# Kernel optimization log

Measured on AMD Instinct MI355X. Metric: run time of the kernel, lower is better.

## Reference

```python
import jax, jax.numpy as jnp
import numpy as np
import math

EPS = 1e-5
NUM_HEADS = 8

def _ln(x, g, b):
    m = x.mean(-1, keepdims=True)
    v = ((x - m) ** 2).mean(-1, keepdims=True)
    return (x - m) / jnp.sqrt(v + EPS) * g + b

def _swish(x):
    return x * jax.nn.sigmoid(x)

def _rope(x):
    # lucidrains RotaryEmbedding.rotate_queries_or_keys: rotates along axis -2,
    # interleaved pair convention, base 10000.
    n, d = x.shape[-2], x.shape[-1]
    inv = 1.0 / (10000.0 ** (jnp.arange(0, d, 2, dtype=jnp.float32) / d))
    freqs = jnp.arange(n, dtype=jnp.float32)[:, None] * inv[None, :]  # (n, d/2)
    cos = jnp.repeat(jnp.cos(freqs), 2, axis=-1)  # (n, d)
    sin = jnp.repeat(jnp.sin(freqs), 2, axis=-1)
    x1, x2 = x[..., 0::2], x[..., 1::2]
    rot = jnp.stack([-x2, x1], axis=-1).reshape(x.shape)
    return x * cos + rot * sin

def _ffn(x, w1, b1, w2, b2):
    # FeedForwardModule: x + 0.5 * (Linear -> Swish -> Linear)
    return x + 0.5 * (_swish(x @ w1 + b1) @ w2 + b2)

def _mhsa(x, g, b, wq, bq, wk, bk, wv, bv, wo, bo):
    B, T, D = x.shape
    dh = D // NUM_HEADS
    y = _ln(x, g, b)
    q = (y @ wq + bq).reshape(B, T, NUM_HEADS, dh)                         # (b,t,h,d)
    k = (y @ wk + bk).reshape(B, T, NUM_HEADS, dh).transpose(0, 2, 1, 3)   # (b,h,t,d)
    v = (y @ wv + bv).reshape(B, T, NUM_HEADS, dh).transpose(0, 2, 1, 3)
    # Faithful to source: query is NOT permuted before rotary, so RoPE acts on
    # axis -2 which is heads for q and time for k (matches torch code exactly).
    q = _rope(q).transpose(0, 2, 1, 3)                                     # (b,h,t,d)
    k = _rope(k)
    score = jnp.einsum('bhtd,bhsd->bhts', q, k) / math.sqrt(D)             # /sqrt(d_model)
    attn = jax.nn.softmax(score, axis=-1)
    ctx = jnp.einsum('bhts,bhsd->bhtd', attn, v).transpose(0, 2, 1, 3).reshape(B, T, D)
    return x + ctx @ wo + bo

def _conv_module(x, g, b, pw1_w, pw1_b, dw_w, dw_b, bn_g, bn_b, pw2_w, pw2_b):
    C = dw_w.shape[-1]  # 2*dim
    y = _ln(x, g, b)
    y = jnp.einsum('btd,ed->bte', y, pw1_w) + pw1_b            # pointwise conv (b,t,4*dim)
    a, gate = y[..., :C], y[..., C:]
    y = a * jax.nn.sigmoid(gate)                                # GLU over channel dim
    y = jax.lax.conv_general_dilated(
        y, dw_w, window_strides=(1,), padding='SAME',
        dimension_numbers=('NWC', 'WIO', 'NWC'), feature_group_count=C) + dw_b
    m = y.mean(axis=(0, 1))                                     # BatchNorm1d, training stats
    v = ((y - m) ** 2).mean(axis=(0, 1))
    y = (y - m) / jnp.sqrt(v + EPS) * bn_g + bn_b
    y = _swish(y)
    y = jnp.einsum('btc,dc->btd', y, pw2_w) + pw2_b             # pointwise conv back to dim
    return x + y

def setup_inputs():
    key = jax.random.key(0)
    B, T, D, K = 8, 1024, 512, 31
    HID = 2 * D
    C = 2 * D
    ks = jax.random.split(key, 16)
    rn = lambda k, shp: jax.random.normal(k, shp, jnp.float32) * 0.02
    zeros = lambda n: jnp.zeros((n,), jnp.float32)
    ones = lambda n: jnp.ones((n,), jnp.float32)
    return dict(
        x=jax.random.normal(ks[0], (B, T, D), jnp.float32),
        ffn1_w1=rn(ks[1], (D, HID)), ffn1_b1=zeros(HID),
        ffn1_w2=rn(ks[2], (HID, D)), ffn1_b2=zeros(D),
        ln_attn_g=ones(D), ln_attn_b=zeros(D),
        wq=rn(ks[3], (D, D)), bq=zeros(D),
        wk=rn(ks[4], (D, D)), bk=zeros(D),
        wv=rn(ks[5], (D, D)), bv=zeros(D),
        wo=rn(ks[6], (D, D)), bo=zeros(D),
        conv_ln_g=ones(D), conv_ln_b=zeros(D),
        pw1_w=rn(ks[7], (2 * C, D)), pw1_b=zeros(2 * C),
        dw_w=rn(ks[8], (K, 1, C)), dw_b=zeros(C),
        bn_g=ones(C), bn_b=zeros(C),
        pw2_w=rn(ks[9], (D, C)), pw2_b=zeros(D),
        ffn2_w1=rn(ks[10], (D, HID)), ffn2_b1=zeros(HID),
        ffn2_w2=rn(ks[11], (HID, D)), ffn2_b2=zeros(D),
        ln_out_g=ones(D), ln_out_b=zeros(D),
    )

def reference(x, ffn1_w1, ffn1_b1, ffn1_w2, ffn1_b2, ln_attn_g, ln_attn_b,
              wq, bq, wk, bk, wv, bv, wo, bo,
              conv_ln_g, conv_ln_b, pw1_w, pw1_b, dw_w, dw_b, bn_g, bn_b, pw2_w, pw2_b,
              ffn2_w1, ffn2_b1, ffn2_w2, ffn2_b2, ln_out_g, ln_out_b):
    y = _ffn(x, ffn1_w1, ffn1_b1, ffn1_w2, ffn1_b2)
    y = _mhsa(y, ln_attn_g, ln_attn_b, wq, bq, wk, bk, wv, bv, wo, bo)
    y = _conv_module(y, conv_ln_g, conv_ln_b, pw1_w, pw1_b, dw_w, dw_b, bn_g, bn_b, pw2_w, pw2_b)
    y = _ffn(y, ffn2_w1, ffn2_b1, ffn2_w2, ffn2_b2)
    return _ln(y, ln_out_g, ln_out_b)
```

## Files before the change

### kernel.cpp

```cpp
#include <hip/hip_runtime.h>
#include <hip/hip_bf16.h>


#define M_ROWS 8192

using bf16x8 = __attribute__((ext_vector_type(8))) short;
using f32x4  = __attribute__((ext_vector_type(4))) float;
using s8v    = __attribute__((ext_vector_type(8))) short;
using s4v    = __attribute__((ext_vector_type(4))) short;

__device__ __forceinline__ float sigmoid_(float v) { return 1.f / (1.f + expf(-v)); }

__device__ __forceinline__ float bf2f(short s) {
  return __uint_as_float(((unsigned)(unsigned short)s) << 16);
}
__device__ __forceinline__ short f2bf(float f) {
  unsigned u = __float_as_uint(f);
  unsigned r = (u + 0x7fffu + ((u >> 16) & 1u)) >> 16;
  return (short)r;
}

__device__ __forceinline__ void gl16(const void* g, void* l) {
  __builtin_amdgcn_global_load_lds((const __attribute__((address_space(1))) void*)g,
                                   (__attribute__((address_space(3))) void*)l, 16, 0, 0);
}

template <int BM, int BN, int BK, int EPI>
__global__ __launch_bounds__(256) void mgemm(
    const short* __restrict__ A, const short* __restrict__ Bt,
    const float* __restrict__ bias, const float* __restrict__ res,
    const short* __restrict__ resb, short* __restrict__ outb, int M, int N, int K) {
  constexpr int WR = BM / 64;
  constexpr int WC = 4 / WR;
  constexpr int NF = BN / (16 * WC);
  constexpr int KH = BK / 32;
  constexpr int APASS = (BM * BK) / 2048;
  constexpr int BPASS = (BN * BK) / 2048;
  constexpr int RPP = 2048 / BK;
  constexpr int LPS = APASS + BPASS;
  __shared__ __align__(16) short As[2][BM * BK];
  __shared__ __align__(16) short Bs[2][BN * BK];
  __shared__ __align__(16) short vstg[EPI == 4 ? 64 * 132 : 1];
  const int tid = threadIdx.x;
  const int lane = tid & 63, wid = tid >> 6;
  const int wr = wid / WC, wc = wid % WC;
  const int nbx = gridDim.x;
  const int nwg = nbx * gridDim.y;
  int id = blockIdx.y * nbx + blockIdx.x;
  id = (id & 7) * (nwg >> 3) + (id >> 3);
  const int bm = (id / nbx) * BM;
  const int bn = (id % nbx) * BN;
  f32x4 acc[4][NF];
#pragma unroll
  for (int m = 0; m < 4; ++m)
#pragma unroll
    for (int n = 0; n < NF; ++n) acc[m][n] = (f32x4){0.f, 0.f, 0.f, 0.f};
  const short* Ablk = A + (size_t)bm * K;
  const short* Bblk = Bt + (size_t)bn * K;
  const int jl = tid & (BK / 8 - 1);
  const int r0 = tid / (BK / 8);
  const int ks = ((BK == 64) ? (jl ^ (r0 & 7)) : jl) << 3;
#define STAGE(buf, k0)                                                                 \
  do {                                                                                 \
    _Pragma("unroll")                                                                  \
    for (int p = 0; p < APASS; ++p)                                                    \
      gl16(Ablk + (size_t)(r0 + p * RPP) * K + (k0) + ks,                              \
           (char*)As[buf] + p * 4096 + wid * 1024);                                    \
    _Pragma("unroll")                                                                  \
    for (int p = 0; p < BPASS; ++p)                                                    \
      gl16(Bblk + (size_t)(r0 + p * RPP) * K + (k0) + ks,                              \
           (char*)Bs[buf] + p * 4096 + wid * 1024);                                    \
  } while (0)

  STAGE(0, 0);
  STAGE(1, BK);
  const int NS = K / BK;
  const int fr = lane & 15, fg = lane >> 4;
  const int arow = wr * 64 + fr;
  const int brow = wc * (BN / WC) + fr;
  for (int i = 0; i < NS; ++i) {
    if (i + 1 < NS) {
      if constexpr (LPS == 4)      asm volatile("s_waitcnt vmcnt(4)" ::: "memory");
      else if constexpr (LPS == 3) asm volatile("s_waitcnt vmcnt(3)" ::: "memory");
      else                         asm volatile("s_waitcnt vmcnt(2)" ::: "memory");
    } else {
      asm volatile("s_waitcnt vmcnt(0)" ::: "memory");
    }
    __builtin_amdgcn_s_barrier();
    asm volatile("" ::: "memory");
    const int cur = i & 1;
    bf16x8 af[KH][4], bfr[KH][NF];
#pragma unroll
    for (int kk = 0; kk < KH; ++kk) {
      const int cx = (BK == 64) ? (((((kk << 2) + fg)) ^ (fr & 7)) << 3)
                                : ((fg << 3) + kk * 32);
#pragma unroll
      for (int m = 0; m < 4; ++m)
        af[kk][m] = *reinterpret_cast<const bf16x8*>(&As[cur][(arow + m * 16) * BK + cx]);
#pragma unroll
      for (int n = 0; n < NF; ++n)
        bfr[kk][n] = *reinterpret_cast<const bf16x8*>(&Bs[cur][(brow + n * 16) * BK + cx]);
    }
    asm volatile("s_waitcnt lgkmcnt(0)" ::: "memory");
    __builtin_amdgcn_s_barrier();
    if ((i + 2) * BK < K) STAGE(cur, (i + 2) * BK);
#pragma unroll
    for (int kk = 0; kk < KH; ++kk)
#pragma unroll
      for (int m = 0; m < 4; ++m)
#pragma unroll
        for (int n = 0; n < NF; ++n)
          acc[m][n] = __builtin_amdgcn_mfma_f32_16x16x32_bf16(af[kk][m], bfr[kk][n],
                                                              acc[m][n], 0, 0, 0);
  }
#undef STAGE
  const int orow0 = bm + wr * 64 + ((lane >> 4) << 2);
  const int ocol0 = bn + wc * (BN / WC) + fr;

  if constexpr (EPI == 4) {
    const int sel = bn >> 9;
    const float2* tbl = (const float2*)res;
    if (sel == 2) {
      const int b_ = bm >> 10, t0v = bm & 1023;
      const int hb = (bn & 511) >> 6;
#pragma unroll
      for (int pass = 0; pass < 2; ++pass) {
        __syncthreads();
        if (wc == pass) {
#pragma unroll
          for (int m = 0; m < 4; ++m) {
            const int rl = wr * 64 + ((lane >> 4) << 2) + m * 16;
#pragma unroll
            for (int n = 0; n < NF; ++n) {
              const int dl = fr + n * 16;
              const float bv = bias[bn + wc * 64 + dl];
#pragma unroll
              for (int r = 0; r < 4; ++r)
                vstg[dl * 132 + rl + r] = f2bf(acc[m][n][r] + bv);
            }
          }
        }
        __syncthreads();
#pragma unroll
        for (int it = 0; it < 4; ++it) {
          const int c = tid + (it << 8);
          const int d = c >> 4, t8 = (c & 15) << 3;
          const s8v val = *reinterpret_cast<const s8v*>(&vstg[d * 132 + t8]);
          *reinterpret_cast<s8v*>(
              &outb[(size_t)8388608 + (((size_t)((b_ << 3) + hb + pass)) << 16) +
                    ((size_t)d << 10) + t0v + t8]) = val;
        }
      }
    } else {
      const float qsc = (sel == 0) ? 0.04419417382415922f : 1.f;
#pragma unroll
      for (int n = 0; n < NF; ++n) {
        const int col = ocol0 + n * 16;
        const int h = (col >> 6) & 7, d = col & 63;
        const int p = d >> 1;
        const float bv = bias[col];
#pragma unroll
        for (int m = 0; m < 4; ++m) {
#pragma unroll
          for (int r = 0; r < 4; ++r) {
            const int row = orow0 + m * 16 + r;
            const int b_ = row >> 10, t_ = row & 1023;
            const int pos = (sel == 0) ? h : t_;
            const float2 cs = tbl[pos * 32 + p];
            float vv = acc[m][n][r] + bv;
            const float pv = __shfl_xor(vv, 1);
            float o = ((lane & 1) == 0) ? (vv * cs.x - pv * cs.y) : (vv * cs.x + pv * cs.y);
            outb[(size_t)sel * 4194304 + (((size_t)((b_ << 3) + h)) << 16) + ((size_t)t_ << 6) + d] =
                f2bf(o * qsc);
          }
        }
      }
    }
  } else if constexpr (EPI == 6) {
    const int j = bn >> 7;
#pragma unroll
    for (int m = 0; m < 4; ++m) {
#pragma unroll
      for (int np = 0; np < NF / 2; ++np) {
        const int gc = (j << 6) + ((wc * 2 + np) << 4) + fr;
        const float ba = bias[gc];
        const float bg = bias[1024 + gc];
#pragma unroll
        for (int r = 0; r < 4; ++r) {
          const int row = orow0 + m * 16 + r;
          const float a = acc[m][2 * np][r] + ba;
          const float g = acc[m][2 * np + 1][r] + bg;
          outb[(size_t)row * 1024 + gc] = f2bf(a * sigmoid_(g));
        }
      }
    }
  } else {
#pragma unroll
    for (int m = 0; m < 4; ++m) {
#pragma unroll
      for (int n = 0; n < NF; ++n) {
        const int col = ocol0 + n * 16;
        const float bv = bias[col];
#pragma unroll
        for (int r = 0; r < 4; ++r) {
          const int row = orow0 + m * 16 + r;
          float v = acc[m][n][r] + bv;
          if constexpr (EPI == 1) {
            v = v * sigmoid_(v);
          } else if constexpr (EPI == 2) {
            v += bf2f(resb[(size_t)row * N + col]);
          } else if constexpr (EPI == 3) {
            v = bf2f(resb[(size_t)row * N + col]) + 0.5f * v;
          }
          outb[(size_t)row * N + col] = f2bf(v);
        }
      }
    }
  }
}

__device__ __forceinline__ void dev_cast8(const float* in, short* out, int i) {
  const float4 a = *reinterpret_cast<const float4*>(&in[(size_t)i * 8]);
  const float4 b = *reinterpret_cast<const float4*>(&in[(size_t)i * 8 + 4]);
  s8v o = { f2bf(a.x), f2bf(a.y), f2bf(a.z), f2bf(a.w),
            f2bf(b.x), f2bf(b.y), f2bf(b.z), f2bf(b.w) };
  *reinterpret_cast<s8v*>(&out[(size_t)i * 8]) = o;
}

__global__ __launch_bounds__(256) void prep_kernel(
    const float* __restrict__ x, short* __restrict__ xb,
    const float* __restrict__ f1w1, short* __restrict__ wf1w1,
    const float* __restrict__ f1w2, short* __restrict__ wf1w2,
    const float* __restrict__ wq, const float* __restrict__ wk,
    const float* __restrict__ wv, short* __restrict__ wqkv,
    const float* __restrict__ wo, short* __restrict__ wwo,
    const float* __restrict__ pw1, short* __restrict__ wpw1,
    const float* __restrict__ pw2, short* __restrict__ wpw2,
    const float* __restrict__ f2w1, short* __restrict__ wf2w1,
    const float* __restrict__ f2w2, short* __restrict__ wf2w2,
    const float* __restrict__ bq, const float* __restrict__ bk,
    const float* __restrict__ bv, float* __restrict__ bqkv,
    float* __restrict__ rtbl) {
  __shared__ float t[32][33];
  const int blk = blockIdx.x, tid = threadIdx.x;
  const float* tin = nullptr;
  short* tout = nullptr;
  int tK = 0, tN = 0, tr = 0, tnbx = 0;
  if (blk < 2048) {
    dev_cast8(x, xb, blk * 256 + tid);
    return;
  } else if (blk < 2560) { tin = f1w1; tout = wf1w1; tK = 512; tN = 1024; tr = blk - 2048; tnbx = 32; }
  else if (blk < 3072)   { tin = f1w2; tout = wf1w2; tK = 1024; tN = 512; tr = blk - 2560; tnbx = 16; }
  else if (blk < 3328)   { tin = wq; tout = wqkv; tK = 512; tN = 512; tr = blk - 3072; tnbx = 16; }
  else if (blk < 3584)   { tin = wk; tout = wqkv + 512 * 512; tK = 512; tN = 512; tr = blk - 3328; tnbx = 16; }
  else if (blk < 3840)   { tin = wv; tout = wqkv + 1024 * 512; tK = 512; tN = 512; tr = blk - 3584; tnbx = 16; }
  else if (blk < 4096)   { tin = wo; tout = wwo; tK = 512; tN = 512; tr = blk - 3840; tnbx = 16; }
  else if (blk < 4608) {
    const int idx = (blk - 4096) * 256 + tid;
    const int pc = idx >> 6, kk = (idx & 63) << 3;
    const int j = pc >> 7, s = (pc >> 4) & 7, fr = pc & 15;
    const int oc = ((s & 1) << 10) + (j << 6) + ((s >> 1) << 4) + fr;
    const float4 a = *reinterpret_cast<const float4*>(&pw1[(size_t)oc * 512 + kk]);
    const float4 b = *reinterpret_cast<const float4*>(&pw1[(size_t)oc * 512 + kk + 4]);
    s8v o = { f2bf(a.x), f2bf(a.y), f2bf(a.z), f2bf(a.w),
              f2bf(b.x), f2bf(b.y), f2bf(b.z), f2bf(b.w) };
    *reinterpret_cast<s8v*>(&wpw1[(size_t)pc * 512 + kk]) = o;
    return;
  } else if (blk < 4864) {
    dev_cast8(pw2, wpw2, (blk - 4608) * 256 + tid);
    return;
  } else if (blk < 5376) { tin = f2w1; tout = wf2w1; tK = 512; tN = 1024; tr = blk - 4864; tnbx = 32; }
  else if (blk < 5888)   { tin = f2w2; tout = wf2w2; tK = 1024; tN = 512; tr = blk - 5376; tnbx = 16; }
  else if (blk < 6016) {
    const int i = (blk - 5888) * 256 + tid;
    const int tt = i >> 5, p = i & 31;
    const float inv = exp2f(-(float)p * 0.41524101186092f);
    float s, c;
    sincosf((float)tt * inv, &s, &c);
    rtbl[i * 2] = c;
    rtbl[i * 2 + 1] = s;
    return;
  } else {
    const int i = (blk - 6016) * 256 + tid;
    if (i < 1536) bqkv[i] = i < 512 ? bq[i] : (i < 1024 ? bk[i - 512] : bv[i - 1024]);
    return;
  }
  const int n0 = (tr % tnbx) << 5, k0 = (tr / tnbx) << 5;
  const int tx = tid & 31, ty = tid >> 5;
  for (int r = ty; r < 32; r += 8) t[r][tx] = tin[(size_t)(k0 + r) * tN + n0 + tx];
  __syncthreads();
  for (int r = ty; r < 32; r += 8) tout[(size_t)(n0 + r) * tK + k0 + tx] = f2bf(t[tx][r]);
}

template <typename OT>
__global__ __launch_bounds__(256) void ln_kernel(
    const short* __restrict__ in, const float* __restrict__ g,
    const float* __restrict__ b, OT* __restrict__ out) {
  __shared__ float sm[4];
  const size_t row = blockIdx.x;
  const int tid = threadIdx.x;
  const short* x = in + (row << 9);
  const int pr = *reinterpret_cast<const int*>(&x[tid << 1]);
  const float v0 = bf2f((short)(pr & 0xffff));
  const float v1 = bf2f((short)(((unsigned)pr) >> 16));
  float s = v0 + v1;
  for (int o = 32; o; o >>= 1) s += __shfl_xor(s, o);
  if ((tid & 63) == 0) sm[tid >> 6] = s;
  __syncthreads();
  const float mean = (sm[0] + sm[1] + sm[2] + sm[3]) * (1.f / 512.f);
  __syncthreads();
  const float d0 = v0 - mean, d1 = v1 - mean;
  float q = d0 * d0 + d1 * d1;
  for (int o = 32; o; o >>= 1) q += __shfl_xor(q, o);
  if ((tid & 63) == 0) sm[tid >> 6] = q;
  __syncthreads();
  const float var = (sm[0] + sm[1] + sm[2] + sm[3]) * (1.f / 512.f);
  const float inv = rsqrtf(var + 1e-5f);
  const float2 gv = *reinterpret_cast<const float2*>(&g[tid << 1]);
  const float2 bv = *reinterpret_cast<const float2*>(&b[tid << 1]);
  const float o0 = d0 * inv * gv.x + bv.x;
  const float o1 = d1 * inv * gv.y + bv.y;
  if constexpr (sizeof(OT) == 2) {
    const int pk = (int)(unsigned short)f2bf(o0) | ((int)(unsigned short)f2bf(o1) << 16);
    *reinterpret_cast<int*>(&out[(row << 9) + (tid << 1)]) = pk;
  } else {
    float2 o = {o0, o1};
    *reinterpret_cast<float2*>(&out[(row << 9) + (tid << 1)]) = o;
  }
}

__global__ __launch_bounds__(256) void attn_mfma_kernel(
    const short* __restrict__ q, const short* __restrict__ k,
    const short* __restrict__ vt, short* __restrict__ ctx) {
  __shared__ __align__(16) short Qs[64][72];
  __shared__ __align__(16) short Ks[64][72];
  __shared__ __align__(16) short VsT[64][72];
  __shared__ __align__(16) short Ps[64][72];
  const int bx = ((blockIdx.x & 7) << 7) | (blockIdx.x >> 3);
  const int bh = bx >> 4, qt = bx & 15;
  const int b_ = bh >> 3, h_ = bh & 7;
  const int tid = threadIdx.x, lane = tid & 63, w = tid >> 6;
  const int t0 = qt << 6;
  const short* qbase = q + ((size_t)bh << 16) + ((size_t)t0 << 6);
  const short* kbase = k + ((size_t)bh << 16);
  const short* vtbase = vt + ((size_t)bh << 16);
  const int sr = tid >> 2, scg = (tid & 3) << 4;
  {
    const s8v a = *reinterpret_cast<const s8v*>(&qbase[(size_t)sr * 64 + scg]);
    const s8v b = *reinterpret_cast<const s8v*>(&qbase[(size_t)sr * 64 + scg + 8]);
    *reinterpret_cast<s8v*>(&Qs[sr][scg]) = a;
    *reinterpret_cast<s8v*>(&Qs[sr][scg + 8]) = b;
    const s8v k0a = *reinterpret_cast<const s8v*>(&kbase[(size_t)sr * 64 + scg]);
    const s8v k0b = *reinterpret_cast<const s8v*>(&kbase[(size_t)sr * 64 + scg + 8]);
    *reinterpret_cast<s8v*>(&Ks[sr][scg]) = k0a;
    *reinterpret_cast<s8v*>(&Ks[sr][scg + 8]) = k0b;
    const s8v v0a = *reinterpret_cast<const s8v*>(&vtbase[((size_t)sr << 10) + scg]);
    const s8v v0b = *reinterpret_cast<const s8v*>(&vtbase[((size_t)sr << 10) + scg + 8]);
    *reinterpret_cast<s8v*>(&VsT[sr][scg]) = v0a;
    *reinterpret_cast<s8v*>(&VsT[sr][scg + 8]) = v0b;
  }
  __syncthreads();
  const int fr = lane & 15, fg = lane >> 4;
  const int koff0 = fg << 3;
  bf16x8 qf[2];
  qf[0] = *reinterpret_cast<const bf16x8*>(&Qs[w * 16 + fr][koff0]);
  qf[1] = *reinterpret_cast<const bf16x8*>(&Qs[w * 16 + fr][32 + koff0]);
  float m[4] = {-1e30f, -1e30f, -1e30f, -1e30f};
  float l[4] = {0.f, 0.f, 0.f, 0.f};
  f32x4 outv[4];
#pragma unroll
  for (int n = 0; n < 4; ++n) outv[n] = (f32x4){0.f, 0.f, 0.f, 0.f};

  for (int i = 0; i < 16; ++i) {
    s8v nk0, nk1, nv0, nv1;
    const bool pf = (i < 15);
    if (pf) {
      const int kn = (i + 1) << 6;
      nk0 = *reinterpret_cast<const s8v*>(&kbase[(size_t)(kn + sr) * 64 + scg]);
      nk1 = *reinterpret_cast<const s8v*>(&kbase[(size_t)(kn + sr) * 64 + scg + 8]);
      nv0 = *reinterpret_cast<const s8v*>(&vtbase[((size_t)sr << 10) + kn + scg]);
      nv1 = *reinterpret_cast<const s8v*>(&vtbase[((size_t)sr << 10) + kn + scg + 8]);
    }
    f32x4 sacc[4];
    __builtin_amdgcn_s_setprio(1);
#pragma unroll
    for (int n = 0; n < 4; ++n) {
      sacc[n] = (f32x4){0.f, 0.f, 0.f, 0.f};
      const bf16x8 kf0 = *reinterpret_cast<const bf16x8*>(&Ks[n * 16 + fr][koff0]);
      const bf16x8 kf1 = *reinterpret_cast<const bf16x8*>(&Ks[n * 16 + fr][32 + koff0]);
      sacc[n] = __builtin_amdgcn_mfma_f32_16x16x32_bf16(qf[0], kf0, sacc[n], 0, 0, 0);
      sacc[n] = __builtin_amdgcn_mfma_f32_16x16x32_bf16(qf[1], kf1, sacc[n], 0, 0, 0);
    }
    __builtin_amdgcn_s_setprio(0);
    float vm[4];
#pragma unroll
    for (int r = 0; r < 4; ++r)
      vm[r] = fmaxf(fmaxf(sacc[0][r], sacc[1][r]), fmaxf(sacc[2][r], sacc[3][r]));
    const bool ok = vm[0] <= m[0] + 8.f && vm[1] <= m[1] + 8.f &&
                    vm[2] <= m[2] + 8.f && vm[3] <= m[3] + 8.f;
    if (__all(ok)) {
#pragma unroll
      for (int r = 0; r < 4; ++r) {
        const float p0 = __expf(sacc[0][r] - m[r]), p1 = __expf(sacc[1][r] - m[r]);
        const float p2 = __expf(sacc[2][r] - m[r]), p3 = __expf(sacc[3][r] - m[r]);
        l[r] += p0 + p1 + p2 + p3;
        const int qr = w * 16 + (fg << 2) + r;
        Ps[qr][fr] = f2bf(p0);
        Ps[qr][16 + fr] = f2bf(p1);
        Ps[qr][32 + fr] = f2bf(p2);
        Ps[qr][48 + fr] = f2bf(p3);
      }
    } else {
#pragma unroll
      for (int r = 0; r < 4; ++r) {
        float rm = vm[r];
        rm = fmaxf(rm, __shfl_xor(rm, 1));
        rm = fmaxf(rm, __shfl_xor(rm, 2));
        rm = fmaxf(rm, __shfl_xor(rm, 4));
        rm = fmaxf(rm, __shfl_xor(rm, 8));
        const float nm = fmaxf(m[r], rm);
        const float al = __expf(m[r] - nm);
        m[r] = nm;
        const float p0 = __expf(sacc[0][r] - nm), p1 = __expf(sacc[1][r] - nm);
        const float p2 = __expf(sacc[2][r] - nm), p3 = __expf(sacc[3][r] - nm);
        l[r] = l[r] * al + (p0 + p1 + p2 + p3);
        outv[0][r] *= al; outv[1][r] *= al; outv[2][r] *= al; outv[3][r] *= al;
        const int qr = w * 16 + (fg << 2) + r;
        Ps[qr][fr] = f2bf(p0);
        Ps[qr][16 + fr] = f2bf(p1);
        Ps[qr][32 + fr] = f2bf(p2);
        Ps[qr][48 + fr] = f2bf(p3);
      }
    }
    __syncthreads();
    if (pf) {
      *reinterpret_cast<s8v*>(&Ks[sr][scg]) = nk0;
      *reinterpret_cast<s8v*>(&Ks[sr][scg + 8]) = nk1;
    }
    const bf16x8 pa0 = *reinterpret_cast<const bf16x8*>(&Ps[w * 16 + fr][koff0]);
    const bf16x8 pa1 = *reinterpret_cast<const bf16x8*>(&Ps[w * 16 + fr][32 + koff0]);
    __builtin_amdgcn_s_setprio(1);
#pragma unroll
    for (int n = 0; n < 4; ++n) {
      const bf16x8 vf0 = *reinterpret_cast<const bf16x8*>(&VsT[n * 16 + fr][koff0]);
      const bf16x8 vf1 = *reinterpret_cast<const bf16x8*>(&VsT[n * 16 + fr][32 + koff0]);
      outv[n] = __builtin_amdgcn_mfma_f32_16x16x32_bf16(pa0, vf0, outv[n], 0, 0, 0);
      outv[n] = __builtin_amdgcn_mfma_f32_16x16x32_bf16(pa1, vf1, outv[n], 0, 0, 0);
    }
    __builtin_amdgcn_s_setprio(0);
    __syncthreads();
    if (pf) {
      *reinterpret_cast<s8v*>(&VsT[sr][scg]) = nv0;
      *reinterpret_cast<s8v*>(&VsT[sr][scg + 8]) = nv1;
    }
  }
#pragma unroll
  for (int r = 0; r < 4; ++r) {
    float L = l[r];
    L += __shfl_xor(L, 1);
    L += __shfl_xor(L, 2);
    L += __shfl_xor(L, 4);
    L += __shfl_xor(L, 8);
    const float inv = 1.f / L;
    const int t = t0 + w * 16 + (fg << 2) + r;
    const size_t base = (((size_t)((b_ << 10) | t)) << 9) + (h_ << 6);
#pragma unroll
    for (int n = 0; n < 4; ++n)
      ctx[base + n * 16 + fr] = f2bf(outv[n][r] * inv);
  }
}

__global__ __launch_bounds__(256) void dwconv_kernel(
    const short* __restrict__ in, const float* __restrict__ w,
    const float* __restrict__ bias, short* __restrict__ out) {
  __shared__ __align__(16) short tile[286 * 72];
  __shared__ float wlds[31 * 64];
  const int id = blockIdx.x;
  const int ct = id & 15, tt = (id >> 4) & 3;
  const size_t b = id >> 6;
  const int c0 = ct << 6, t0 = tt << 8;
  const int tid = threadIdx.x;
  for (int i = tid; i < 31 * 64; i += 256) {
    const int kk = i >> 6, c = i & 63;
    wlds[i] = w[kk * 1024 + c0 + c];
  }
  for (int i = tid; i < 286 * 8; i += 256) {
    const int row = i >> 3, seg = i & 7;
    const int gt = t0 - 15 + row;
    s8v val = {};
    if (gt >= 0 && gt < 1024)
      val = *reinterpret_cast<const s8v*>(&in[(b << 20) + ((size_t)gt << 10) + c0 + (seg << 3)]);
    *reinterpret_cast<s8v*>(&tile[row * 72 + (seg << 3)]) = val;
  }
  __syncthreads();
  const int cg = tid & 7, tg = tid >> 3;
  const int tl = tg << 3;
  float acc[8][8];
  const float4 b0 = *reinterpret_cast<const float4*>(&bias[c0 + (cg << 3)]);
  const float4 b1 = *reinterpret_cast<const float4*>(&bias[c0 + (cg << 3) + 4]);
#pragma unroll
  for (int t = 0; t < 8; ++t) {
    acc[t][0] = b0.x; acc[t][1] = b0.y; acc[t][2] = b0.z; acc[t][3] = b0.w;
    acc[t][4] = b1.x; acc[t][5] = b1.y; acc[t][6] = b1.z; acc[t][7] = b1.w;
  }
  for (int kk = 0; kk < 31; ++kk) {
    const float4 w0 = *reinterpret_cast<const float4*>(&wlds[kk * 64 + (cg << 3)]);
    const float4 w1 = *reinterpret_cast<const float4*>(&wlds[kk * 64 + (cg << 3) + 4]);
#pragma unroll
    for (int t = 0; t < 8; ++t) {
      const s8v xv = *reinterpret_cast<const s8v*>(&tile[(tl + t + kk) * 72 + (cg << 3)]);
      acc[t][0] = fmaf(bf2f(xv[0]), w0.x, acc[t][0]);
      acc[t][1] = fmaf(bf2f(xv[1]), w0.y, acc[t][1]);
      acc[t][2] = fmaf(bf2f(xv[2]), w0.z, acc[t][2]);
      acc[t][3] = fmaf(bf2f(xv[3]), w0.w, acc[t][3]);
      acc[t][4] = fmaf(bf2f(xv[4]), w1.x, acc[t][4]);
      acc[t][5] = fmaf(bf2f(xv[5]), w1.y, acc[t][5]);
      acc[t][6] = fmaf(bf2f(xv[6]), w1.z, acc[t][6]);
      acc[t][7] = fmaf(bf2f(xv[7]), w1.w, acc[t][7]);
    }
  }
#pragma unroll
  for (int t = 0; t < 8; ++t) {
    s8v o;
#pragma unroll
    for (int j = 0; j < 8; ++j) o[j] = f2bf(acc[t][j]);
    *reinterpret_cast<s8v*>(&out[(b << 20) + ((size_t)(t0 + tl + t) << 10) + c0 + (cg << 3)]) = o;
  }
}

__global__ __launch_bounds__(256) void bn_stats_kernel(
    const short* __restrict__ y, float* __restrict__ ps, float* __restrict__ pq) {
  const int tid = threadIdx.x;
  const int c4 = tid << 2;
  const size_t r0 = (size_t)blockIdx.x * 32;
  float s[4] = {0, 0, 0, 0}, q[4] = {0, 0, 0, 0};
  for (int r = 0; r < 32; ++r) {
    const s4v v = *reinterpret_cast<const s4v*>(&y[((r0 + r) << 10) + c4]);
#pragma unroll
    for (int j = 0; j < 4; ++j) {
      const float f = bf2f(v[j]);
      s[j] += f;
      q[j] = fmaf(f, f, q[j]);
    }
  }
#pragma unroll
  for (int j = 0; j < 4; ++j) {
    ps[(size_t)blockIdx.x * 1024 + c4 + j] = s[j];
    pq[(size_t)blockIdx.x * 1024 + c4 + j] = q[j];
  }
}

__global__ __launch_bounds__(256) void bn_finalize_kernel(
    const float* __restrict__ ps, const float* __restrict__ pq, float* __restrict__ stats) {
  const int c = blockIdx.x * 256 + threadIdx.x;
  float s = 0.f, q = 0.f;
  for (int i = 0; i < 256; ++i) {
    s += ps[i * 1024 + c];
    q += pq[i * 1024 + c];
  }
  const float mean = s * (1.f / 8192.f);
  const float var = q * (1.f / 8192.f) - mean * mean;
  stats[c] = mean;
  stats[1024 + c] = rsqrtf(fmaxf(var, 0.f) + 1e-5f);
}

__global__ __launch_bounds__(256) void bn_apply_kernel(
    const short* __restrict__ y, const float* __restrict__ g, const float* __restrict__ b,
    const float* __restrict__ stats, short* __restrict__ out) {
  const size_t i = (size_t)blockIdx.x * 256 + threadIdx.x;
  const size_t f = i << 2;
  const int c = (int)(f & 1023);
  const s4v yv = *reinterpret_cast<const s4v*>(&y[f]);
  s4v o;
#pragma unroll
  for (int j = 0; j < 4; ++j) {
    const float v = (bf2f(yv[j]) - stats[c + j]) * stats[1024 + c + j] * g[c + j] + b[c + j];
    o[j] = f2bf(v * sigmoid_(v));
  }
  *reinterpret_cast<s4v*>(&out[f]) = o;
}

extern "C" void kernel_launch(void* const* d_in, const int* in_sizes, int n_in,
                              void* d_out, int out_size, void* d_ws, size_t ws_size,
                              hipStream_t stream) {
  const float* x        = (const float*)d_in[0];
  const float* ffn1_w1  = (const float*)d_in[1];
  const float* ffn1_b1  = (const float*)d_in[2];
  const float* ffn1_w2  = (const float*)d_in[3];
  const float* ffn1_b2  = (const float*)d_in[4];
  const float* ln_att_g = (const float*)d_in[5];
  const float* ln_att_b = (const float*)d_in[6];
  const float* wq       = (const float*)d_in[7];
  const float* bq       = (const float*)d_in[8];
  const float* wk       = (const float*)d_in[9];
  const float* bk       = (const float*)d_in[10];
  const float* wv       = (const float*)d_in[11];
  const float* bv       = (const float*)d_in[12];
  const float* wo_      = (const float*)d_in[13];
  const float* bo       = (const float*)d_in[14];
  const float* cln_g    = (const float*)d_in[15];
  const float* cln_b    = (const float*)d_in[16];
  const float* pw1_w    = (const float*)d_in[17];
  const float* pw1_b    = (const float*)d_in[18];
  const float* dw_w     = (const float*)d_in[19];
  const float* dw_b     = (const float*)d_in[20];
  const float* bn_g     = (const float*)d_in[21];
  const float* bn_b     = (const float*)d_in[22];
  const float* pw2_w    = (const float*)d_in[23];
  const float* pw2_b    = (const float*)d_in[24];
  const float* ffn2_w1  = (const float*)d_in[25];
  const float* ffn2_b1  = (const float*)d_in[26];
  const float* ffn2_w2  = (const float*)d_in[27];
  const float* ffn2_b2  = (const float*)d_in[28];
  const float* ln_out_g = (const float*)d_in[29];
  const float* ln_out_b = (const float*)d_in[30];

  char* wsb = (char*)d_ws;
  const size_t MB = 1u << 20;
  short* buf_y = (short*)(wsb);
  char* Bre = wsb + 16 * MB;
  short* qkv16 = (short*)(Bre);
  short* lnq  = (short*)(Bre + 48 * MB);
  short* ctx  = (short*)(Bre + 56 * MB);
  short* h1   = (short*)(Bre);
  short* xb   = (short*)(Bre + 16 * MB);
  short* gluo = (short*)(Bre);
  short* bno  = (short*)(Bre + 48 * MB);
  char* Cre = wsb + 80 * MB;
  short* lnc  = (short*)(Cre);
  short* dwo16= (short*)(Cre + 8 * MB);
  char* Dre = wsb + 112 * MB;
  short* w_f1w1 = (short*)(Dre);
  short* w_f1w2 = (short*)(Dre + 1 * MB);
  short* w_qkv  = (short*)(Dre + 2 * MB);
  short* w_wo   = (short*)(Dre + 3 * MB + 512 * 1024);
  short* w_pw1  = (short*)(Dre + 4 * MB);
  short* w_pw2  = (short*)(Dre + 6 * MB);
  short* w_f2w1 = (short*)(Dre + 7 * MB);
  short* w_f2w2 = (short*)(Dre + 8 * MB);
  float* bqkv   = (float*)(Dre + 9 * MB);
  float* ps     = (float*)(Dre + 9 * MB + 8192);
  float* pq     = (float*)(Dre + 10 * MB + 8192);
  float* stats  = (float*)(Dre + 11 * MB + 8192);
  float* rtbl   = (float*)(Dre + 12 * MB);

  const dim3 blk(256);

  prep_kernel<<<6022, blk, 0, stream>>>(
      x, xb, ffn1_w1, w_f1w1, ffn1_w2, w_f1w2, wq, wk, wv, w_qkv, wo_, w_wo,
      pw1_w, w_pw1, pw2_w, w_pw2, ffn2_w1, w_f2w1, ffn2_w2, w_f2w2,
      bq, bk, bv, bqkv, rtbl);

  mgemm<64, 64, 64, 1><<<dim3(16, 128), blk, 0, stream>>>(xb, w_f1w1, ffn1_b1, nullptr, nullptr, h1, M_ROWS, 1024, 512);
  mgemm<64, 64, 64, 3><<<dim3(8, 128), blk, 0, stream>>>(h1, w_f1w2, ffn1_b2, nullptr, xb, buf_y, M_ROWS, 512, 1024);

  ln_kernel<short><<<M_ROWS, blk, 0, stream>>>(buf_y, ln_att_g, ln_att_b, lnq);
  mgemm<128, 128, 32, 4><<<dim3(12, 64), blk, 0, stream>>>(lnq, w_qkv, bqkv, rtbl, nullptr, qkv16, M_ROWS, 1536, 512);
  attn_mfma_kernel<<<1024, blk, 0, stream>>>(qkv16, qkv16 + 4194304, qkv16 + 8388608, ctx);
  mgemm<64, 64, 64, 2><<<dim3(8, 128), blk, 0, stream>>>(ctx, w_wo, bo, nullptr, buf_y, buf_y, M_ROWS, 512, 512);

  ln_kernel<short><<<M_ROWS, blk, 0, stream>>>(buf_y, cln_g, cln_b, lnc);
  mgemm<128, 128, 32, 6><<<dim3(16, 64), blk, 0, stream>>>(lnc, w_pw1, pw1_b, nullptr, nullptr, gluo, M_ROWS, 2048, 512);
  dwconv_kernel<<<512, blk, 0, stream>>>(gluo, dw_w, dw_b, dwo16);
  bn_stats_kernel<<<256, blk, 0, stream>>>(dwo16, ps, pq);
  bn_finalize_kernel<<<4, blk, 0, stream>>>(ps, pq, stats);
  bn_apply_kernel<<<8192, blk, 0, stream>>>(dwo16, bn_g, bn_b, stats, bno);
  mgemm<64, 64, 64, 2><<<dim3(8, 128), blk, 0, stream>>>(bno, w_pw2, pw2_b, nullptr, buf_y, buf_y, M_ROWS, 512, 1024);

  mgemm<64, 64, 64, 1><<<dim3(16, 128), blk, 0, stream>>>(buf_y, w_f2w1, ffn2_b1, nullptr, nullptr, h1, M_ROWS, 1024, 512);
  mgemm<64, 64, 64, 3><<<dim3(8, 128), blk, 0, stream>>>(h1, w_f2w2, ffn2_b2, nullptr, buf_y, buf_y, M_ROWS, 512, 1024);

  ln_kernel<float><<<M_ROWS, blk, 0, stream>>>(buf_y, ln_out_g, ln_out_b, (float*)d_out);
}
```

Measured before the change: 286.8 us.

## Process two query tiles per attention block to reuse K/V tiles

Each attention workgroup now handles 128 query rows, as two 64-row sub-tiles, instead of 64, so every K and V tile loaded into LDS is used twice. This halves the grid to 512 blocks and halves global K/V traffic. The Q staging buffer is folded into the double P buffer. The price is more registers per thread and fewer blocks to fill the GPU. f2bf is also switched to the library __float2bfloat16 conversion.

```diff
diff --git a/kernel.cpp b/kernel.cpp
--- a/kernel.cpp
+++ b/kernel.cpp
@@ -15,9 +15,8 @@
   return __uint_as_float(((unsigned)(unsigned short)s) << 16);
 }
 __device__ __forceinline__ short f2bf(float f) {
-  unsigned u = __float_as_uint(f);
-  unsigned r = (u + 0x7fffu + ((u >> 16) & 1u)) >> 16;
-  return (short)r;
+  __hip_bfloat16 h = __float2bfloat16(f);
+  return *reinterpret_cast<short*>(&h);
 }
 
 __device__ __forceinline__ void gl16(const void* g, void* l) {
@@ -332,24 +331,26 @@
 __global__ __launch_bounds__(256) void attn_mfma_kernel(
     const short* __restrict__ q, const short* __restrict__ k,
     const short* __restrict__ vt, short* __restrict__ ctx) {
-  __shared__ __align__(16) short Qs[64][72];
   __shared__ __align__(16) short Ks[64][72];
   __shared__ __align__(16) short VsT[64][72];
-  __shared__ __align__(16) short Ps[64][72];
-  const int bx = ((blockIdx.x & 7) << 7) | (blockIdx.x >> 3);
-  const int bh = bx >> 4, qt = bx & 15;
+  __shared__ __align__(16) short Ps[2][64][72];
+  const int bx = ((blockIdx.x & 7) << 6) | (blockIdx.x >> 3);
+  const int bh = bx >> 3, qt = bx & 7;
   const int b_ = bh >> 3, h_ = bh & 7;
   const int tid = threadIdx.x, lane = tid & 63, w = tid >> 6;
-  const int t0 = qt << 6;
+  const int t0 = qt << 7;
   const short* qbase = q + ((size_t)bh << 16) + ((size_t)t0 << 6);
   const short* kbase = k + ((size_t)bh << 16);
   const short* vtbase = vt + ((size_t)bh << 16);
   const int sr = tid >> 2, scg = (tid & 3) << 4;
+  short* Qtmp = &Ps[0][0][0];
   {
-    const s8v a = *reinterpret_cast<const s8v*>(&qbase[(size_t)sr * 64 + scg]);
-    const s8v b = *reinterpret_cast<const s8v*>(&qbase[(size_t)sr * 64 + scg + 8]);
-    *reinterpret_cast<s8v*>(&Qs[sr][scg]) = a;
-    *reinterpret_cast<s8v*>(&Qs[sr][scg + 8]) = b;
+    const int sr2 = tid >> 1, sc2 = (tid & 1) << 5;
+#pragma unroll
+    for (int j = 0; j < 4; ++j) {
+      const s8v v = *reinterpret_cast<const s8v*>(&qbase[(size_t)sr2 * 64 + sc2 + j * 8]);
+      *reinterpret_cast<s8v*>(&Qtmp[sr2 * 72 + sc2 + j * 8]) = v;
+    }
     const s8v k0a = *reinterpret_cast<const s8v*>(&kbase[(size_t)sr * 64 + scg]);
     const s8v k0b = *reinterpret_cast<const s8v*>(&kbase[(size_t)sr * 64 + scg + 8]);
     *reinterpret_cast<s8v*>(&Ks[sr][scg]) = k0a;
@@ -362,14 +363,23 @@
   __syncthreads();
   const int fr = lane & 15, fg = lane >> 4;
   const int koff0 = fg << 3;
-  bf16x8 qf[2];
-  qf[0] = *reinterpret_cast<const bf16x8*>(&Qs[w * 16 + fr][koff0]);
-  qf[1] = *reinterpret_cast<const bf16x8*>(&Qs[w * 16 + fr][32 + koff0]);
-  float m[4] = {-1e30f, -1e30f, -1e30f, -1e30f};
-  float l[4] = {0.f, 0.f, 0.f, 0.f};
-  f32x4 outv[4];
-#pragma unroll
-  for (int n = 0; n < 4; ++n) outv[n] = (f32x4){0.f, 0.f, 0.f, 0.f};
+  bf16x8 qf[2][2];
+#pragma unroll
+  for (int a = 0; a < 2; ++a) {
+    qf[a][0] = *reinterpret_cast<const bf16x8*>(&Qtmp[(a * 64 + w * 16 + fr) * 72 + koff0]);
+    qf[a][1] = *reinterpret_cast<const bf16x8*>(&Qtmp[(a * 64 + w * 16 + fr) * 72 + 32 + koff0]);
+  }
+  __syncthreads();
+  float m[2][4], l[2][4];
+  f32x4 outv[2][4];
+#pragma unroll
+  for (int a = 0; a < 2; ++a)
+#pragma unroll
+    for (int r = 0; r < 4; ++r) { m[a][r] = -1e30f; l[a][r] = 0.f; }
+#pragma unroll
+  for (int a = 0; a < 2; ++a)
+#pragma unroll
+    for (int n = 0; n < 4; ++n) outv[a][n] = (f32x4){0.f, 0.f, 0.f, 0.f};
 
   for (int i = 0; i < 16; ++i) {
     s8v nk0, nk1, nv0, nv1;
@@ -381,71 +391,86 @@
       nv0 = *reinterpret_cast<const s8v*>(&vtbase[((size_t)sr << 10) + kn + scg]);
       nv1 = *reinterpret_cast<const s8v*>(&vtbase[((size_t)sr << 10) + kn + scg + 8]);
     }
-    f32x4 sacc[4];
+    f32x4 sacc[2][4];
     __builtin_amdgcn_s_setprio(1);
 #pragma unroll
     for (int n = 0; n < 4; ++n) {
-      sacc[n] = (f32x4){0.f, 0.f, 0.f, 0.f};
       const bf16x8 kf0 = *reinterpret_cast<const bf16x8*>(&Ks[n * 16 + fr][koff0]);
       const bf16x8 kf1 = *reinterpret_cast<const bf16x8*>(&Ks[n * 16 + fr][32 + koff0]);
-      sacc[n] = __builtin_amdgcn_mfma_f32_16x16x32_bf16(qf[0], kf0, sacc[n], 0, 0, 0);
-      sacc[n] = __builtin_amdgcn_mfma_f32_16x16x32_bf16(qf[1], kf1, sacc[n], 0, 0, 0);
+#pragma unroll
+      for (int a = 0; a < 2; ++a) {
+        sacc[a][n] = (f32x4){0.f, 0.f, 0.f, 0.f};
+        sacc[a][n] = __builtin_amdgcn_mfma_f32_16x16x32_bf16(qf[a][0], kf0, sacc[a][n], 0, 0, 0);
+        sacc[a][n] = __builtin_amdgcn_mfma_f32_16x16x32_bf16(qf[a][1], kf1, sacc[a][n], 0, 0, 0);
+      }
     }
     __builtin_amdgcn_s_setprio(0);
-    float vm[4];
-#pragma unroll
-    for (int r = 0; r < 4; ++r)
-      vm[r] = fmaxf(fmaxf(sacc[0][r], sacc[1][r]), fmaxf(sacc[2][r], sacc[3][r]));
-    const bool ok = vm[0] <= m[0] + 8.f && vm[1] <= m[1] + 8.f &&
-                    vm[2] <= m[2] + 8.f && vm[3] <= m[3] + 8.f;
+    float vm[2][4];
+    bool ok = true;
+#pragma unroll
+    for (int a = 0; a < 2; ++a)
+#pragma unroll
+      for (int r = 0; r < 4; ++r) {
+        vm[a][r] = fmaxf(fmaxf(sacc[a][0][r], sacc[a][1][r]),
+                         fmaxf(sacc[a][2][r], sacc[a][3][r]));
+        ok = ok && (vm[a][r] <= m[a][r] + 8.f);
+      }
     if (__all(ok)) {
 #pragma unroll
-      for (int r = 0; r < 4; ++r) {
-        const float p0 = __expf(sacc[0][r] - m[r]), p1 = __expf(sacc[1][r] - m[r]);
-        const float p2 = __expf(sacc[2][r] - m[r]), p3 = __expf(sacc[3][r] - m[r]);
-        l[r] += p0 + p1 + p2 + p3;
-        const int qr = w * 16 + (fg << 2) + r;
-        Ps[qr][fr] = f2bf(p0);
-        Ps[qr][16 + fr] = f2bf(p1);
-        Ps[qr][32 + fr] = f2bf(p2);
-        Ps[qr][48 + fr] = f2bf(p3);
-      }
+      for (int a = 0; a < 2; ++a)
+#pragma unroll
+        for (int r = 0; r < 4; ++r) {
+          const float p0 = __expf(sacc[a][0][r] - m[a][r]), p1 = __expf(sacc[a][1][r] - m[a][r]);
+          const float p2 = __expf(sacc[a][2][r] - m[a][r]), p3 = __expf(sacc[a][3][r] - m[a][r]);
+          l[a][r] += p0 + p1 + p2 + p3;
+          const int qr = w * 16 + (fg << 2) + r;
+          Ps[a][qr][fr] = f2bf(p0);
+          Ps[a][qr][16 + fr] = f2bf(p1);
+          Ps[a][qr][32 + fr] = f2bf(p2);
+          Ps[a][qr][48 + fr] = f2bf(p3);
+        }
     } else {
 #pragma unroll
-      for (int r = 0; r < 4; ++r) {
-        float rm = vm[r];
-        rm = fmaxf(rm, __shfl_xor(rm, 1));
-        rm = fmaxf(rm, __shfl_xor(rm, 2));
-        rm = fmaxf(rm, __shfl_xor(rm, 4));
-        rm = fmaxf(rm, __shfl_xor(rm, 8));
-        const float nm = fmaxf(m[r], rm);
-        const float al = __expf(m[r] - nm);
-        m[r] = nm;
-        const float p0 = __expf(sacc[0][r] - nm), p1 = __expf(sacc[1][r] - nm);
-        const float p2 = __expf(sacc[2][r] - nm), p3 = __expf(sacc[3][r] - nm);
-        l[r] = l[r] * al + (p0 + p1 + p2 + p3);
-        outv[0][r] *= al; outv[1][r] *= al; outv[2][r] *= al; outv[3][r] *= al;
-        const int qr = w * 16 + (fg << 2) + r;
-        Ps[qr][fr] = f2bf(p0);
-        Ps[qr][16 + fr] = f2bf(p1);
-        Ps[qr][32 + fr] = f2bf(p2);
-        Ps[qr][48 + fr] = f2bf(p3);
-      }
+      for (int a = 0; a < 2; ++a)
+#pragma unroll
+        for (int r = 0; r < 4; ++r) {
+          float rm = vm[a][r];
+          rm = fmaxf(rm, __shfl_xor(rm, 1));
+          rm = fmaxf(rm, __shfl_xor(rm, 2));
+          rm = fmaxf(rm, __shfl_xor(rm, 4));
+          rm = fmaxf(rm, __shfl_xor(rm, 8));
+          const float nm = fmaxf(m[a][r], rm);
+          const float al = __expf(m[a][r] - nm);
+          m[a][r] = nm;
+          const float p0 = __expf(sacc[a][0][r] - nm), p1 = __expf(sacc[a][1][r] - nm);
+          const float p2 = __expf(sacc[a][2][r] - nm), p3 = __expf(sacc[a][3][r] - nm);
+          l[a][r] = l[a][r] * al + (p0 + p1 + p2 + p3);
+          outv[a][0][r] *= al; outv[a][1][r] *= al;
+          outv[a][2][r] *= al; outv[a][3][r] *= al;
+          const int qr = w * 16 + (fg << 2) + r;
+          Ps[a][qr][fr] = f2bf(p0);
+          Ps[a][qr][16 + fr] = f2bf(p1);
+          Ps[a][qr][32 + fr] = f2bf(p2);
+          Ps[a][qr][48 + fr] = f2bf(p3);
+        }
     }
     __syncthreads();
     if (pf) {
       *reinterpret_cast<s8v*>(&Ks[sr][scg]) = nk0;
       *reinterpret_cast<s8v*>(&Ks[sr][scg + 8]) = nk1;
     }
-    const bf16x8 pa0 = *reinterpret_cast<const bf16x8*>(&Ps[w * 16 + fr][koff0]);
-    const bf16x8 pa1 = *reinterpret_cast<const bf16x8*>(&Ps[w * 16 + fr][32 + koff0]);
     __builtin_amdgcn_s_setprio(1);
 #pragma unroll
-    for (int n = 0; n < 4; ++n) {
-      const bf16x8 vf0 = *reinterpret_cast<const bf16x8*>(&VsT[n * 16 + fr][koff0]);
-      const bf16x8 vf1 = *reinterpret_cast<const bf16x8*>(&VsT[n * 16 + fr][32 + koff0]);
-      outv[n] = __builtin_amdgcn_mfma_f32_16x16x32_bf16(pa0, vf0, outv[n], 0, 0, 0);
-      outv[n] = __builtin_amdgcn_mfma_f32_16x16x32_bf16(pa1, vf1, outv[n], 0, 0, 0);
+    for (int a = 0; a < 2; ++a) {
+      const bf16x8 pa0 = *reinterpret_cast<const bf16x8*>(&Ps[a][w * 16 + fr][koff0]);
+      const bf16x8 pa1 = *reinterpret_cast<const bf16x8*>(&Ps[a][w * 16 + fr][32 + koff0]);
+#pragma unroll
+      for (int n = 0; n < 4; ++n) {
+        const bf16x8 vf0 = *reinterpret_cast<const bf16x8*>(&VsT[n * 16 + fr][koff0]);
+        const bf16x8 vf1 = *reinterpret_cast<const bf16x8*>(&VsT[n * 16 + fr][32 + koff0]);
+        outv[a][n] = __builtin_amdgcn_mfma_f32_16x16x32_bf16(pa0, vf0, outv[a][n], 0, 0, 0);
+        outv[a][n] = __builtin_amdgcn_mfma_f32_16x16x32_bf16(pa1, vf1, outv[a][n], 0, 0, 0);
+      }
     }
     __builtin_amdgcn_s_setprio(0);
     __syncthreads();
@@ -455,19 +480,21 @@
     }
   }
 #pragma unroll
-  for (int r = 0; r < 4; ++r) {
-    float L = l[r];
-    L += __shfl_xor(L, 1);
-    L += __shfl_xor(L, 2);
-    L += __shfl_xor(L, 4);
-    L += __shfl_xor(L, 8);
-    const float inv = 1.f / L;
-    const int t = t0 + w * 16 + (fg << 2) + r;
-    const size_t base = (((size_t)((b_ << 10) | t)) << 9) + (h_ << 6);
-#pragma unroll
-    for (int n = 0; n < 4; ++n)
-      ctx[base + n * 16 + fr] = f2bf(outv[n][r] * inv);
-  }
+  for (int a = 0; a < 2; ++a)
+#pragma unroll
+    for (int r = 0; r < 4; ++r) {
+      float L = l[a][r];
+      L += __shfl_xor(L, 1);
+      L += __shfl_xor(L, 2);
+      L += __shfl_xor(L, 4);
+      L += __shfl_xor(L, 8);
+      const float inv = 1.f / L;
+      const int t = t0 + a * 64 + w * 16 + (fg << 2) + r;
+      const size_t base = (((size_t)((b_ << 10) | t)) << 9) + (h_ << 6);
+#pragma unroll
+      for (int n = 0; n < 4; ++n)
+        ctx[base + n * 16 + fr] = f2bf(outv[a][n][r] * inv);
+    }
 }
 
 __global__ __launch_bounds__(256) void dwconv_kernel(
@@ -656,7 +683,7 @@
 
   ln_kernel<short><<<M_ROWS, blk, 0, stream>>>(buf_y, ln_att_g, ln_att_b, lnq);
   mgemm<128, 128, 32, 4><<<dim3(12, 64), blk, 0, stream>>>(lnq, w_qkv, bqkv, rtbl, nullptr, qkv16, M_ROWS, 1536, 512);
-  attn_mfma_kernel<<<1024, blk, 0, stream>>>(qkv16, qkv16 + 4194304, qkv16 + 8388608, ctx);
+  attn_mfma_kernel<<<512, blk, 0, stream>>>(qkv16, qkv16 + 4194304, qkv16 + 8388608, ctx);
   mgemm<64, 64, 64, 2><<<dim3(8, 128), blk, 0, stream>>>(ctx, w_wo, bo, nullptr, buf_y, buf_y, M_ROWS, 512, 512);
 
   ln_kernel<short><<<M_ROWS, blk, 0, stream>>>(buf_y, cln_g, cln_b, lnc);
```

New measurement: 284.4 us. No clear change (-0.8%).
